# Kernel optimization log

Measured on AMD Instinct MI355X. Metric: run time of the kernel, lower is better.

Reference implementation:

```python
import jax, jax.numpy as jnp
import numpy as np

# CapsuleConv2d(128, 256, 3, in_length=16, out_length=16, stride=1, padding=1,
#               share_weight=True, routing_type='k_means' (dot), num_iterations=3, squash=True)
KH = KW = 3
SH = SW = 1
PH = PW = 1
DH = DW = 1
IN_LENGTH = 16
OUT_LENGTH = 16
NUM_ITERS = 3
EPS = 1e-12


def _extract_patches(x):
    # x: [B, C, H, W] -> [B, C, KH, KW, OH, OW] (torch.nn.functional.unfold layout)
    B, C, H, W = x.shape
    OH = (H + 2 * PH - DH * (KH - 1) - 1) // SH + 1
    OW = (W + 2 * PW - DW * (KW - 1) - 1) // SW + 1
    xp = jnp.pad(x, ((0, 0), (0, 0), (PH, PH), (PW, PW)))
    rows = []
    for i in range(KH):  # small fixed kernel loop
        cols = []
        for j in range(KW):
            cols.append(xp[:, :, i * DH: i * DH + (OH - 1) * SH + 1: SH,
                              j * DW: j * DW + (OW - 1) * SW + 1: SW])
        rows.append(jnp.stack(cols, axis=2))
    return jnp.stack(rows, axis=2)  # [B, C, KH, KW, OH, OW]


def _k_means_routing(u, num_iterations):
    # u: [B, OH, OW, N_in, O, L]; routing over N_in (axis -3), dot similarity
    v = u.mean(axis=-3, keepdims=True)  # [B, OH, OW, 1, O, L]
    for _ in range(num_iterations):
        vn = v / jnp.maximum(jnp.linalg.norm(v, axis=-1, keepdims=True), EPS)
        logits = jnp.sum(u * vn, axis=-1, keepdims=True)      # [B,OH,OW,N_in,O,1]
        probs = jax.nn.softmax(logits, axis=-3)
        v = jnp.sum(probs * u, axis=-3, keepdims=True)
    return jnp.squeeze(v, axis=-3)  # [B, OH, OW, O, L]


def _squash(s):
    norm = jnp.linalg.norm(s, axis=-1, keepdims=True)
    return s * (norm / (1.0 + norm * norm))  # = ||s||^2/(1+||s||^2) * s/||s||


def setup_inputs() -> dict:
    key = jax.random.key(0)
    k1, k2 = jax.random.split(key)
    x = jax.random.normal(k1, (2, 128, 32, 32), dtype=jnp.float32)
    # weight: [O=out_channels//out_length, L=out_length, M=in_length, KH, KW]
    fan = IN_LENGTH * KH * KW + OUT_LENGTH * KH * KW
    bound = float(np.sqrt(6.0 / fan))  # xavier_uniform-ish scale
    weight = jax.random.uniform(k2, (16, 16, 16, 3, 3), dtype=jnp.float32,
                                minval=-bound, maxval=bound)
    return {"x": x, "weight": weight}


def reference(x, weight):
    B = x.shape[0]
    O, L, M = weight.shape[0], weight.shape[1], weight.shape[2]
    patches = _extract_patches(x)                      # [B, C, KH, KW, OH, OW]
    OH, OW = patches.shape[-2], patches.shape[-1]
    G = x.shape[1] // M
    patches = patches.reshape(B, G, M, KH, KW, OH, OW)
    # priors[b,h,w,g,i,j,o,l] = sum_m patch[b,g,m,i,j,h,w] * weight[o,l,m,i,j]
    priors = jnp.einsum('bgmijhw,olmij->bhwgijol', patches, weight)
    priors = priors.reshape(B, OH, OW, G * KH * KW, O, L)
    v = _k_means_routing(priors, NUM_ITERS)            # [B, OH, OW, O, L]
    v = _squash(v)
    out = v.reshape(B, OH, OW, O * L).transpose(0, 3, 1, 2)  # [B, C_out, OH, OW]
    return out
```

## Files before the change

### kernel.cpp

```cpp
#include <hip/hip_runtime.h>


typedef float v2f __attribute__((ext_vector_type(2)));

#define NPRI 72
#define XT_ELEMS (2 * 32 * 32 * 128)
#define WT_ELEMS (9 * 256 * 16)
#define ROWSTR 264

#define DPP_ADD(a, ctrl)                                                     \
  a += __int_as_float(__builtin_amdgcn_update_dpp(                           \
          0, __float_as_int(a), ctrl, 0xF, 0xF, true))

__device__ __forceinline__ float dpp_add16(float x) {
    float s = x;
    DPP_ADD(s, 0x128); DPP_ADD(s, 0x124); DPP_ADD(s, 0x122); DPP_ADD(s, 0x121);
    return s;
}

__device__ __forceinline__ float frcp(float x) {
    return __builtin_amdgcn_rcpf(x);
}

__device__ __forceinline__ v2f pkfma(v2f a, v2f b, v2f c) {
    return __builtin_elementwise_fma(a, b, c);
}

__global__ __launch_bounds__(256)
void prep_kernel(const float* __restrict__ x, const float* __restrict__ W,
                 float* __restrict__ xT, float* __restrict__ Wt) {
    const int blk = blockIdx.x;
    const int tid = threadIdx.x;
    if (blk < 64) {
        __shared__ float xs[128 * 33];
        const int b = blk >> 5, h = blk & 31;
        const float* xb = x + b * (128 * 32 * 32) + h * 32;
        #pragma unroll
        for (int k = 0; k < 16; ++k) {
            int idx = k * 256 + tid;
            int c = idx >> 5, w = idx & 31;
            xs[c * 33 + w] = xb[c * 1024 + w];
        }
        __syncthreads();
        float* xo = xT + (b * 32 + h) * 32 * 128;
        #pragma unroll
        for (int k = 0; k < 16; ++k) {
            int idx = k * 256 + tid;
            int w = idx >> 7, c = idx & 127;
            xo[w * 128 + c] = xs[c * 33 + w];
        }
    } else {
        int idx = (blk - 64) * 256 + tid;
        int ij = idx >> 12;
        int r  = idx & 4095;
        int tt = r >> 4;
        int m  = r & 15;
        Wt[idx] = W[(tt * 16 + m) * 9 + ij];
    }
}

__global__ __launch_bounds__(256, 1)
void capsule_v4(const float* __restrict__ xT, const float* __restrict__ Wt,
                float* __restrict__ out) {
    __shared__ float uTs[36 * ROWSTR];
    const int pix = blockIdx.x;
    const int b = pix >> 10, h = (pix >> 5) & 31, w = pix & 31;
    const int t = threadIdx.x;
    const int o = t >> 4, nc = t & 15;

    float u[NPRI];
    #pragma unroll
    for (int n = 0; n < NPRI; ++n) u[n] = 0.0f;

    #pragma unroll
    for (int ij = 0; ij < 9; ++ij) {
        const int di = ij / 3, dj = ij % 3;
        const int hh = h + di - 1, ww = w + dj - 1;
        if ((unsigned)hh < 32u && (unsigned)ww < 32u) {
            const v2f* sp2 = (const v2f*)(xT + ((b * 32 + hh) * 32 + ww) * 128);
            const v2f* wp2 = (const v2f*)(Wt + (ij * 256 + t) * 16);
            v2f wr2[8];
            #pragma unroll
            for (int m = 0; m < 8; ++m) wr2[m] = wp2[m];
            #pragma unroll
            for (int g = 0; g < 8; ++g) {
                v2f acc = {0.0f, 0.0f};
                #pragma unroll
                for (int m = 0; m < 8; ++m)
                    acc = pkfma(sp2[g * 8 + m], wr2[m], acc);
                u[g * 9 + ij] = acc.x + acc.y;
            }
        }
    }

    v2f ut2[5][8];
    #pragma unroll
    for (int j2 = 0; j2 < 8; ++j2) ut2[4][j2] = (v2f){0.0f, 0.0f};
    const bool has5 = (nc < 8);

    #pragma unroll
    for (int n = 0; n < 36; ++n) uTs[n * ROWSTR + t] = u[n];
    __syncthreads();
    {
        #pragma unroll
        for (int k = 0; k < 2; ++k) {
            const v2f* r2 = (const v2f*)&uTs[(nc + 16 * k) * ROWSTR + o * 16];
            #pragma unroll
            for (int j2 = 0; j2 < 8; ++j2) ut2[k][j2] = r2[j2];
        }
        if (nc < 4) {
            const v2f* r2 = (const v2f*)&uTs[(32 + nc) * ROWSTR + o * 16];
            #pragma unroll
            for (int j2 = 0; j2 < 8; ++j2) ut2[2][j2] = r2[j2];
        }
    }
    __syncthreads();
    #pragma unroll
    for (int n = 36; n < NPRI; ++n) uTs[(n - 36) * ROWSTR + t] = u[n];
    __syncthreads();
    {
        if (nc >= 4) {
            const v2f* r2 = (const v2f*)&uTs[(nc - 4) * ROWSTR + o * 16];
            #pragma unroll
            for (int j2 = 0; j2 < 8; ++j2) ut2[2][j2] = r2[j2];
        }
        {
            const v2f* r2 = (const v2f*)&uTs[(12 + nc) * ROWSTR + o * 16];
            #pragma unroll
            for (int j2 = 0; j2 < 8; ++j2) ut2[3][j2] = r2[j2];
        }
        if (has5) {
            const v2f* r2 = (const v2f*)&uTs[(28 + nc) * ROWSTR + o * 16];
            #pragma unroll
            for (int j2 = 0; j2 < 8; ++j2) ut2[4][j2] = r2[j2];
        }
    }

    v2f va2[8];
    #pragma unroll
    for (int j2 = 0; j2 < 8; ++j2) {
        v2f s = (ut2[0][j2] + ut2[1][j2]) + (ut2[2][j2] + ut2[3][j2]) + ut2[4][j2];
        va2[j2].x = dpp_add16(s.x) * (1.0f / NPRI);
        va2[j2].y = dpp_add16(s.y) * (1.0f / NPRI);
    }

    #pragma unroll 1
    for (int it = 0; it < 3; ++it) {
        v2f ssv = {0.0f, 0.0f};
        #pragma unroll
        for (int j2 = 0; j2 < 8; ++j2) ssv = pkfma(va2[j2], va2[j2], ssv);
        float ss = ssv.x + ssv.y;
        float inv = frcp(fmaxf(sqrtf(ss), 1e-12f));

        float e[5], ssum = 0.0f;
        #pragma unroll
        for (int k = 0; k < 5; ++k) {
            v2f d2 = {0.0f, 0.0f};
            #pragma unroll
            for (int j2 = 0; j2 < 8; ++j2) d2 = pkfma(ut2[k][j2], va2[j2], d2);
            float ek = __expf((d2.x + d2.y) * inv);
            if (k == 4) ek = has5 ? ek : 0.0f;
            e[k] = ek;
            ssum += ek;
        }
        ssum = dpp_add16(ssum);
        float rs = frcp(ssum);

        v2f e0 = {e[0], e[0]}, e1 = {e[1], e[1]}, e2v = {e[2], e[2]};
        v2f e3 = {e[3], e[3]}, e4 = {e[4], e[4]};
        #pragma unroll
        for (int j2 = 0; j2 < 8; ++j2) {
            v2f pv = e0 * ut2[0][j2];
            pv = pkfma(e1, ut2[1][j2], pv);
            pv = pkfma(e2v, ut2[2][j2], pv);
            pv = pkfma(e3, ut2[3][j2], pv);
            pv = pkfma(e4, ut2[4][j2], pv);
            va2[j2].x = dpp_add16(pv.x) * rs;
            va2[j2].y = dpp_add16(pv.y) * rs;
        }
    }

    v2f ssv = {0.0f, 0.0f};
    #pragma unroll
    for (int j2 = 0; j2 < 8; ++j2) ssv = pkfma(va2[j2], va2[j2], ssv);
    float ss = ssv.x + ssv.y;
    float scale = sqrtf(ss) * frcp(1.0f + ss);

    v2f c4[4], c2[2];
    #pragma unroll
    for (int j = 0; j < 4; ++j) c4[j] = (nc & 8) ? va2[j + 4] : va2[j];
    #pragma unroll
    for (int j = 0; j < 2; ++j) c2[j] = (nc & 4) ? c4[j + 2] : c4[j];
    v2f c1 = (nc & 2) ? c2[1] : c2[0];
    float res = ((nc & 1) ? c1.y : c1.x) * scale;

    out[((b * 256 + t) * 32 + h) * 32 + w] = res;
}

__global__ __launch_bounds__(256, 1)
void capsule_fb(const float* __restrict__ x, const float* __restrict__ Wraw,
                float* __restrict__ out) {
    __shared__ float patch[9 * 128];
    const int blk = blockIdx.x;
    const int b = blk >> 10, h = (blk >> 5) & 31, w = blk & 31;
    const int t = threadIdx.x;

    const float* xb = x + b * (128 * 32 * 32);
    for (int idx = t; idx < 1152; idx += 256) {
        int c = idx / 9, ij = idx - c * 9;
        int di = ij / 3, dj = ij - di * 3;
        int hh = h + di - 1, ww = w + dj - 1;
        float v = 0.0f;
        if ((unsigned)hh < 32u && (unsigned)ww < 32u)
            v = xb[(c * 32 + hh) * 32 + ww];
        patch[ij * 128 + c] = v;
    }
    __syncthreads();

    float u[NPRI];
    #pragma unroll
    for (int ij = 0; ij < 9; ++ij) {
        float wr[16];
        #pragma unroll
        for (int m = 0; m < 16; ++m) wr[m] = Wraw[(t * 16 + m) * 9 + ij];
        #pragma unroll
        for (int g = 0; g < 8; ++g) {
            float acc = 0.0f;
            #pragma unroll
            for (int m = 0; m < 16; ++m)
                acc = fmaf(patch[ij * 128 + g * 16 + m], wr[m], acc);
            u[g * 9 + ij] = acc;
        }
    }

    float v = 0.0f;
    #pragma unroll
    for (int n = 0; n < NPRI; ++n) v += u[n];
    v *= (1.0f / NPRI);
    #pragma unroll 1
    for (int it = 0; it < 3; ++it) {
        float s = dpp_add16(v * v);
        float vn = v * frcp(fmaxf(sqrtf(s), 1e-12f));
        float ssum = 0.0f, vacc = 0.0f;
        #pragma unroll
        for (int n = 0; n < NPRI; ++n) {
            float p = dpp_add16(u[n] * vn);
            float e = __expf(p);
            ssum += e;
            vacc = fmaf(e, u[n], vacc);
        }
        v = vacc * frcp(ssum);
    }
    float s = dpp_add16(v * v);
    float res = v * sqrtf(s) * frcp(1.0f + s);
    out[((b * 256 + t) * 32 + h) * 32 + w] = res;
}

extern "C" void kernel_launch(void* const* d_in, const int* in_sizes, int n_in,
                              void* d_out, int out_size, void* d_ws, size_t ws_size,
                              hipStream_t stream) {
    const float* x = (const float*)d_in[0];
    const float* W = (const float*)d_in[1];
    float* out = (float*)d_out;
    float* xT = (float*)d_ws;
    float* Wt = xT + XT_ELEMS;

    const size_t need = (size_t)(XT_ELEMS + WT_ELEMS) * sizeof(float);
    if (ws_size >= need) {
        prep_kernel<<<208, 256, 0, stream>>>(x, W, xT, Wt);
        capsule_v4<<<2048, 256, 0, stream>>>(xT, Wt, out);
    } else {
        capsule_fb<<<2048, 256, 0, stream>>>(x, W, out);
    }
}
```

Measured before the change: 97.18 us.

## Split prior computation into two halves written directly to LDS to raise occupancy

Drops the 72-float per-thread prior array and computes the priors in two passes of four capsule groups each, storing each result straight into the shared transpose buffer between barriers. This lowers register pressure so the launch bound can ask for three blocks per CU instead of one. The LDS row stride is also padded differently to change the bank mapping. In exchange, each of the nine neighbour weight rows is loaded twice, and out-of-bounds taps now have to write explicit zeros.

```diff
diff --git a/kernel.cpp b/kernel.cpp
--- a/kernel.cpp
+++ b/kernel.cpp
@@ -6,7 +6,7 @@
 #define NPRI 72
 #define XT_ELEMS (2 * 32 * 32 * 128)
 #define WT_ELEMS (9 * 256 * 16)
-#define ROWSTR 264
+#define ROWSTR 268
 
 #define DPP_ADD(a, ctrl)                                                     \
   a += __int_as_float(__builtin_amdgcn_update_dpp(                           \
@@ -59,8 +59,8 @@
     }
 }
 
-__global__ __launch_bounds__(256, 1)
-void capsule_v4(const float* __restrict__ xT, const float* __restrict__ Wt,
+__global__ __launch_bounds__(256, 3)
+void capsule_v5(const float* __restrict__ xT, const float* __restrict__ Wt,
                 float* __restrict__ out) {
     __shared__ float uTs[36 * ROWSTR];
     const int pix = blockIdx.x;
@@ -68,9 +68,10 @@
     const int t = threadIdx.x;
     const int o = t >> 4, nc = t & 15;
 
-    float u[NPRI];
-    #pragma unroll
-    for (int n = 0; n < NPRI; ++n) u[n] = 0.0f;
+    v2f ut2[5][8];
+    #pragma unroll
+    for (int j2 = 0; j2 < 8; ++j2) ut2[4][j2] = (v2f){0.0f, 0.0f};
+    const bool has5 = (nc < 8);
 
     #pragma unroll
     for (int ij = 0; ij < 9; ++ij) {
@@ -83,23 +84,19 @@
             #pragma unroll
             for (int m = 0; m < 8; ++m) wr2[m] = wp2[m];
             #pragma unroll
-            for (int g = 0; g < 8; ++g) {
+            for (int g = 0; g < 4; ++g) {
                 v2f acc = {0.0f, 0.0f};
                 #pragma unroll
                 for (int m = 0; m < 8; ++m)
                     acc = pkfma(sp2[g * 8 + m], wr2[m], acc);
-                u[g * 9 + ij] = acc.x + acc.y;
+                uTs[(g * 9 + ij) * ROWSTR + t] = acc.x + acc.y;
             }
-        }
-    }
-
-    v2f ut2[5][8];
-    #pragma unroll
-    for (int j2 = 0; j2 < 8; ++j2) ut2[4][j2] = (v2f){0.0f, 0.0f};
-    const bool has5 = (nc < 8);
-
-    #pragma unroll
-    for (int n = 0; n < 36; ++n) uTs[n * ROWSTR + t] = u[n];
+        } else {
+            #pragma unroll
+            for (int g = 0; g < 4; ++g)
+                uTs[(g * 9 + ij) * ROWSTR + t] = 0.0f;
+        }
+    }
     __syncthreads();
     {
         #pragma unroll
@@ -115,8 +112,31 @@
         }
     }
     __syncthreads();
-    #pragma unroll
-    for (int n = 36; n < NPRI; ++n) uTs[(n - 36) * ROWSTR + t] = u[n];
+
+    #pragma unroll
+    for (int ij = 0; ij < 9; ++ij) {
+        const int di = ij / 3, dj = ij % 3;
+        const int hh = h + di - 1, ww = w + dj - 1;
+        if ((unsigned)hh < 32u && (unsigned)ww < 32u) {
+            const v2f* sp2 = (const v2f*)(xT + ((b * 32 + hh) * 32 + ww) * 128);
+            const v2f* wp2 = (const v2f*)(Wt + (ij * 256 + t) * 16);
+            v2f wr2[8];
+            #pragma unroll
+            for (int m = 0; m < 8; ++m) wr2[m] = wp2[m];
+            #pragma unroll
+            for (int g = 0; g < 4; ++g) {
+                v2f acc = {0.0f, 0.0f};
+                #pragma unroll
+                for (int m = 0; m < 8; ++m)
+                    acc = pkfma(sp2[(g + 4) * 8 + m], wr2[m], acc);
+                uTs[(g * 9 + ij) * ROWSTR + t] = acc.x + acc.y;
+            }
+        } else {
+            #pragma unroll
+            for (int g = 0; g < 4; ++g)
+                uTs[(g * 9 + ij) * ROWSTR + t] = 0.0f;
+        }
+    }
     __syncthreads();
     {
         if (nc >= 4) {
@@ -268,7 +288,7 @@
     const size_t need = (size_t)(XT_ELEMS + WT_ELEMS) * sizeof(float);
     if (ws_size >= need) {
         prep_kernel<<<208, 256, 0, stream>>>(x, W, xT, Wt);
-        capsule_v4<<<2048, 256, 0, stream>>>(xT, Wt, out);
+        capsule_v5<<<2048, 256, 0, stream>>>(xT, Wt, out);
     } else {
         capsule_fb<<<2048, 256, 0, stream>>>(x, W, out);
     }
```

Result: slower. 107.2 us (+10.3%).
